# Performance work log

Hardware: AMD Instinct MI355X
Metric: run time of the kernel (lower is better)

The kernel has to match this reference:

```python
import jax, jax.numpy as jnp
import numpy as np

N_NODES = 100000
N_EDGES = 1600000
DIM_IN = 128
DIM_OUT = 64


def _spmm(edge_row, edge_col, edge_vals, X):
    # DAD.mm(X): sparse COO [N,N] times dense [N,d]
    # gather source features, scale by edge value, scatter-add to rows
    msgs = edge_vals[:, None] * X[edge_col]          # [E, d]
    return jax.ops.segment_sum(msgs, edge_row, num_segments=N_NODES)


def setup_inputs() -> dict:
    key = jax.random.key(0)
    k1, k2, k3, k4, k5, k6 = jax.random.split(key, 6)
    X = jax.random.normal(k1, (N_NODES, DIM_IN), dtype=jnp.float32)
    W1 = jax.random.normal(k2, (DIM_IN, DIM_IN), dtype=jnp.float32) * (1.0 / np.sqrt(DIM_IN))
    W2 = jax.random.normal(k3, (DIM_OUT, DIM_IN), dtype=jnp.float32) * (1.0 / np.sqrt(DIM_IN))
    edge_vals = jax.random.uniform(k4, (N_EDGES,), dtype=jnp.float32)
    edge_row = jax.random.randint(k5, (N_EDGES,), 0, N_NODES, dtype=jnp.int32)
    edge_col = jax.random.randint(k6, (N_EDGES,), 0, N_NODES, dtype=jnp.int32)
    return {"X": X, "W1": W1, "W2": W2, "edge_vals": edge_vals,
            "edge_row": edge_row, "edge_col": edge_col}


def reference(X, W1, W2, edge_vals, edge_row, edge_col):
    # layer 1: tanh(fc1(DAD @ X)); nn.Linear(bias=False) is x @ W.T
    h = jnp.tanh(_spmm(edge_row, edge_col, edge_vals, X) @ W1.T)
    # layer 2: tanh(fc2(DAD @ h))
    out = jnp.tanh(_spmm(edge_row, edge_col, edge_vals, h) @ W2.T)
    return out
```

## Files before the change

### kernel.cpp

```cpp
#include <hip/hip_runtime.h>
#include <hip/hip_bf16.h>
#include <hip/hip_fp16.h>

#define N_NODES 100000
#define N_EDGES 1600000
#define DIM_IN 128
#define DIM_OUT 64

#define NB 391
#define NCHUNK 391
#define CHUNK 4096
#define BCAP 5120

typedef unsigned int uint;
typedef unsigned short ushort;
typedef _Float16 half8 __attribute__((ext_vector_type(8)));
typedef float f32x4 __attribute__((ext_vector_type(4)));

__device__ inline ushort f2h(float f) {
    __half h = __float2half(f);
    return *reinterpret_cast<ushort*>(&h);
}


__global__ __launch_bounds__(256) void chunk_hist_kernel(const int* __restrict__ erow,
                                                         int* __restrict__ counts, int E) {
    __shared__ int hist[NB];
    const int t = threadIdx.x, c = blockIdx.x;
    for (int b = t; b < NB; b += 256) hist[b] = 0;
    __syncthreads();
    const int eb = c * CHUNK;
#pragma unroll
    for (int i = 0; i < CHUNK / 256; ++i) {
        int e = eb + i * 256 + t;
        if (e < E) atomicAdd(&hist[erow[e] >> 8], 1);
    }
    __syncthreads();
    for (int b = t; b < NB; b += 256) counts[b * NCHUNK + c] = hist[b];
}

__global__ __launch_bounds__(512) void bucket_scan_kernel(const int* __restrict__ counts,
                                                          int* __restrict__ offnb,
                                                          int* __restrict__ tot) {
    __shared__ int s[512];
    const int b = blockIdx.x, t = threadIdx.x;
    int v = (t < NCHUNK) ? counts[b * NCHUNK + t] : 0;
    s[t] = v;
    __syncthreads();
#pragma unroll
    for (int o = 1; o < 512; o <<= 1) {
        int x = s[t];
        int y = (t >= o) ? s[t - o] : 0;
        __syncthreads();
        s[t] = x + y;
        __syncthreads();
    }
    if (t < NCHUNK) offnb[b * NCHUNK + t] = s[t] - v;
    if (t == 511) tot[b] = s[511];
}

__global__ __launch_bounds__(512) void base_scan_kernel(const int* __restrict__ tot,
                                                        int* __restrict__ bbase) {
    __shared__ int s[512];
    const int t = threadIdx.x;
    int v = (t < NB) ? tot[t] : 0;
    s[t] = v;
    __syncthreads();
#pragma unroll
    for (int o = 1; o < 512; o <<= 1) {
        int x = s[t];
        int y = (t >= o) ? s[t - o] : 0;
        __syncthreads();
        s[t] = x + y;
        __syncthreads();
    }
    if (t < NB) bbase[t] = s[t] - v;
    if (t == 511) bbase[NB] = s[511];
}

__global__ __launch_bounds__(512) void coarse_scatter_kernel(const int* __restrict__ erow,
                                                             const int* __restrict__ ecol,
                                                             const float* __restrict__ eval,
                                                             const int* __restrict__ offnb,
                                                             const int* __restrict__ bbase,
                                                             uint* __restrict__ keyOut,
                                                             float* __restrict__ valOut, int E) {
    __shared__ int hist[NB];
    __shared__ int segOff[NB];
    __shared__ int localOff[NB];
    __shared__ int sc[512];
    __shared__ int idxL[CHUNK];
    __shared__ int gaddrL[CHUNK];

    const int t = threadIdx.x, c = blockIdx.x;
    for (int b = t; b < NB; b += 512) {
        hist[b] = 0;
        segOff[b] = bbase[b] + offnb[b * NCHUNK + c];
    }
    __syncthreads();
    const int eb = c * CHUNK;
    uint bq[CHUNK / 512];
#pragma unroll
    for (int i = 0; i < CHUNK / 512; ++i) {
        int e = eb + i * 512 + t;
        if (e < E) {
            int b = erow[e] >> 8;
            int q = atomicAdd(&hist[b], 1);
            bq[i] = ((uint)b << 16) | (uint)q;
        } else {
            bq[i] = 0xFFFFFFFFu;
        }
    }
    __syncthreads();
    int v = (t < NB) ? hist[t] : 0;
    sc[t] = v;
    __syncthreads();
#pragma unroll
    for (int o = 1; o < 512; o <<= 1) {
        int x = sc[t];
        int y = (t >= o) ? sc[t - o] : 0;
        __syncthreads();
        sc[t] = x + y;
        __syncthreads();
    }
    if (t < NB) localOff[t] = sc[t] - v;
    __syncthreads();
#pragma unroll
    for (int i = 0; i < CHUNK / 512; ++i) {
        if (bq[i] != 0xFFFFFFFFu) {
            int b = bq[i] >> 16;
            int q = bq[i] & 0xFFFF;
            int s = localOff[b] + q;
            idxL[s] = eb + i * 512 + t;
            gaddrL[s] = segOff[b] + q;
        }
    }
    __syncthreads();
    const int m = min(CHUNK, E - eb);
    for (int s = t; s < m; s += 512) {
        int e = idxL[s];
        int g = gaddrL[s];
        keyOut[g] = ((uint)(erow[e] & 255) << 17) | (uint)ecol[e];
        valOut[g] = eval[e];
    }
}

__global__ __launch_bounds__(256) void fine_sort_kernel(const uint* __restrict__ keyOut,
                                                        const float* __restrict__ valOut,
                                                        const int* __restrict__ bbase,
                                                        int* __restrict__ row_ptr,
                                                        int2* __restrict__ ep) {
    __shared__ uint keyL[BCAP];
    __shared__ int hist[256];
    __shared__ int offs[256];
    const int b = blockIdx.x, t = threadIdx.x;
    const int s0 = bbase[b], s1 = bbase[b + 1];
    const int m = min(s1 - s0, BCAP);
    hist[t] = 0;
    __syncthreads();
    for (int j = t; j < m; j += 256) {
        uint k = keyOut[s0 + j];
        keyL[j] = k;
        atomicAdd(&hist[k >> 17], 1);
    }
    __syncthreads();
    int v = hist[t];
    offs[t] = v;
    __syncthreads();
#pragma unroll
    for (int o = 1; o < 256; o <<= 1) {
        int x = offs[t];
        int y = (t >= o) ? offs[t - o] : 0;
        __syncthreads();
        offs[t] = x + y;
        __syncthreads();
    }
    int excl = offs[t] - v;
    int row = b * 256 + t;
    if (row < N_NODES) row_ptr[row] = s0 + excl;
    if (b == NB - 1 && t == 0) row_ptr[N_NODES] = s1;
    hist[t] = excl;
    __syncthreads();
    for (int j = t; j < m; j += 256) {
        uint k = keyL[j];
        int pos = atomicAdd(&hist[k >> 17], 1);
        float vv = valOut[s0 + j];
        ep[s0 + pos] = make_int2((int)(k & 0x1FFFFu), __float_as_int(vv));
    }
}


__global__ __launch_bounds__(256) void cvt_f16_kernel(const float* __restrict__ in,
                                                      uint* __restrict__ outp, int n8) {
    int i = blockIdx.x * 256 + threadIdx.x;
    if (i >= n8) return;
    const float4* in4 = reinterpret_cast<const float4*>(in) + (size_t)i * 2;
    float4 a = in4[0];
    float4 b = in4[1];
    uint4 o;
    o.x = (uint)f2h(a.x) | ((uint)f2h(a.y) << 16);
    o.y = (uint)f2h(a.z) | ((uint)f2h(a.w) << 16);
    o.z = (uint)f2h(b.x) | ((uint)f2h(b.y) << 16);
    o.w = (uint)f2h(b.z) | ((uint)f2h(b.w) << 16);
    reinterpret_cast<uint4*>(outp)[i] = o;
}


__global__ __launch_bounds__(256) void spmm_f16_kernel(const int2* __restrict__ ep,
                                                       const int* __restrict__ row_ptr,
                                                       const uint* __restrict__ Xh,
                                                       uint* __restrict__ aggh) {
    int wave = threadIdx.x >> 6;
    int lane = threadIdx.x & 63;
    int r = blockIdx.x * 4 + wave;
    if (r >= N_NODES) return;
    int beg = row_ptr[r];
    int end = row_ptr[r + 1];
    float a0x = 0.f, a0y = 0.f, a1x = 0.f, a1y = 0.f;
    int e = beg;
    for (; e + 7 < end; e += 8) {
        int2 cv[8];
        uint xu[8];
#pragma unroll
        for (int i = 0; i < 8; ++i) cv[i] = ep[e + i];
#pragma unroll
        for (int i = 0; i < 8; ++i) xu[i] = Xh[(size_t)cv[i].x * 64 + lane];
#pragma unroll
        for (int i = 0; i < 8; ++i) {
            float v = __int_as_float(cv[i].y);
            __half2 h2 = *reinterpret_cast<__half2*>(&xu[i]);
            float2 f = __half22float2(h2);
            if (i & 1) { a1x += v * f.x; a1y += v * f.y; }
            else       { a0x += v * f.x; a0y += v * f.y; }
        }
    }
    for (; e < end; ++e) {
        int2 cv = ep[e];
        float v = __int_as_float(cv.y);
        uint xu = Xh[(size_t)cv.x * 64 + lane];
        __half2 h2 = *reinterpret_cast<__half2*>(&xu);
        float2 f = __half22float2(h2);
        a0x += v * f.x;
        a0y += v * f.y;
    }
    uint o = (uint)f2h(a0x + a1x) | ((uint)f2h(a0y + a1y) << 16);
    aggh[(size_t)r * 64 + lane] = o;
}


__global__ __launch_bounds__(256) void spmm64_f16_tanh_kernel(const int2* __restrict__ ep,
                                                              const int* __restrict__ row_ptr,
                                                              const ushort* __restrict__ Ph,
                                                              float* __restrict__ out) {
    int wave = threadIdx.x >> 6;
    int lane = threadIdx.x & 63;
    int r = blockIdx.x * 4 + wave;
    if (r >= N_NODES) return;
    int beg = row_ptr[r];
    int end = row_ptr[r + 1];
    float acc0 = 0.f, acc1 = 0.f;
    int e = beg;
    for (; e + 7 < end; e += 8) {
        int2 cv[8];
        ushort xu[8];
#pragma unroll
        for (int i = 0; i < 8; ++i) cv[i] = ep[e + i];
#pragma unroll
        for (int i = 0; i < 8; ++i) xu[i] = Ph[(size_t)cv[i].x * 64 + lane];
#pragma unroll
        for (int i = 0; i < 8; ++i) {
            float v = __int_as_float(cv[i].y);
            __half h = *reinterpret_cast<__half*>(&xu[i]);
            float x = __half2float(h);
            if (i & 1) acc1 += v * x;
            else       acc0 += v * x;
        }
    }
    for (; e < end; ++e) {
        int2 cv = ep[e];
        ushort u = Ph[(size_t)cv.x * 64 + lane];
        __half h = *reinterpret_cast<__half*>(&u);
        acc0 += __int_as_float(cv.y) * __half2float(h);
    }
    out[(size_t)r * DIM_OUT + lane] = tanhf(acc0 + acc1);
}


__global__ __launch_bounds__(256) void fused_mlp_kernel(const uint* __restrict__ Ah,
                                                        const uint* __restrict__ W1h,
                                                        const uint* __restrict__ W2h,
                                                        uint* __restrict__ Ph, int M) {
    __shared__ __align__(16) ushort sA[128 * 128];
    __shared__ __align__(16) ushort sW1[128 * 128];
    __shared__ __align__(16) ushort sW2[64 * 128];

    const int t = threadIdx.x;
    const int l = t & 63;
    const int w = t >> 6;
    const int row0 = blockIdx.x * 128;
    const int lr = l & 15;
    const int lk = l >> 4;

#pragma unroll
    for (int i = 0; i < 8; ++i) {
        int fid = i * 256 + t;
        int row = fid >> 4, slot = fid & 15;
        int gr = row0 + row;
        uint4 v = make_uint4(0, 0, 0, 0);
        if (gr < M) v = reinterpret_cast<const uint4*>(Ah)[(size_t)gr * 16 + slot];
        *reinterpret_cast<uint4*>(&sA[row * 128 + ((slot ^ (row & 7)) << 3)]) = v;
    }
#pragma unroll
    for (int i = 0; i < 8; ++i) {
        int fid = i * 256 + t;
        int row = fid >> 4, slot = fid & 15;
        uint4 v = reinterpret_cast<const uint4*>(W1h)[row * 16 + slot];
        *reinterpret_cast<uint4*>(&sW1[row * 128 + ((slot ^ (row & 7)) << 3)]) = v;
    }
#pragma unroll
    for (int i = 0; i < 4; ++i) {
        int fid = i * 256 + t;
        int row = fid >> 4, slot = fid & 15;
        uint4 v = reinterpret_cast<const uint4*>(W2h)[row * 16 + slot];
        *reinterpret_cast<uint4*>(&sW2[row * 128 + ((slot ^ (row & 7)) << 3)]) = v;
    }
    __syncthreads();

    f32x4 acc[2][8];
#pragma unroll
    for (int rf = 0; rf < 2; ++rf)
#pragma unroll
        for (int cf = 0; cf < 8; ++cf) acc[rf][cf] = (f32x4){0.f, 0.f, 0.f, 0.f};

    half8 aF[2][4];
#pragma unroll
    for (int rf = 0; rf < 2; ++rf) {
        int row = w * 32 + rf * 16 + lr;
#pragma unroll
        for (int kc = 0; kc < 4; ++kc) {
            int slot = kc * 4 + lk;
            aF[rf][kc] = *reinterpret_cast<const half8*>(&sA[row * 128 + ((slot ^ (row & 7)) << 3)]);
        }
    }
#pragma unroll
    for (int cf = 0; cf < 8; ++cf) {
        int col = cf * 16 + lr;
#pragma unroll
        for (int kc = 0; kc < 4; ++kc) {
            int slot = kc * 4 + lk;
            half8 bF = *reinterpret_cast<const half8*>(&sW1[col * 128 + ((slot ^ (col & 7)) << 3)]);
            acc[0][cf] = __builtin_amdgcn_mfma_f32_16x16x32_f16(aF[0][kc], bF, acc[0][cf], 0, 0, 0);
            acc[1][cf] = __builtin_amdgcn_mfma_f32_16x16x32_f16(aF[1][kc], bF, acc[1][cf], 0, 0, 0);
        }
    }
    __syncthreads();

#pragma unroll
    for (int rf = 0; rf < 2; ++rf)
#pragma unroll
        for (int cf = 0; cf < 8; ++cf)
#pragma unroll
            for (int reg = 0; reg < 4; ++reg) {
                int row = w * 32 + rf * 16 + lk * 4 + reg;
                int col = cf * 16 + lr;
                sA[row * 128 + (((col >> 3) ^ (row & 7)) << 3) + (col & 7)] =
                    f2h(tanhf(acc[rf][cf][reg]));
            }
    __syncthreads();

    f32x4 acc2[2][4];
#pragma unroll
    for (int rf = 0; rf < 2; ++rf)
#pragma unroll
        for (int cf = 0; cf < 4; ++cf) acc2[rf][cf] = (f32x4){0.f, 0.f, 0.f, 0.f};
#pragma unroll
    for (int rf = 0; rf < 2; ++rf) {
        int row = w * 32 + rf * 16 + lr;
#pragma unroll
        for (int kc = 0; kc < 4; ++kc) {
            int slot = kc * 4 + lk;
            aF[rf][kc] = *reinterpret_cast<const half8*>(&sA[row * 128 + ((slot ^ (row & 7)) << 3)]);
        }
    }
#pragma unroll
    for (int cf = 0; cf < 4; ++cf) {
        int col = cf * 16 + lr;
#pragma unroll
        for (int kc = 0; kc < 4; ++kc) {
            int slot = kc * 4 + lk;
            half8 bF = *reinterpret_cast<const half8*>(&sW2[col * 128 + ((slot ^ (col & 7)) << 3)]);
            acc2[0][cf] = __builtin_amdgcn_mfma_f32_16x16x32_f16(aF[0][kc], bF, acc2[0][cf], 0, 0, 0);
            acc2[1][cf] = __builtin_amdgcn_mfma_f32_16x16x32_f16(aF[1][kc], bF, acc2[1][cf], 0, 0, 0);
        }
    }

    ushort* sP = sW1;
#pragma unroll
    for (int rf = 0; rf < 2; ++rf)
#pragma unroll
        for (int cf = 0; cf < 4; ++cf)
#pragma unroll
            for (int reg = 0; reg < 4; ++reg) {
                int row = w * 32 + rf * 16 + lk * 4 + reg;
                int col = cf * 16 + lr;
                sP[row * 64 + col] = f2h(acc2[rf][cf][reg]);
            }
    __syncthreads();

#pragma unroll
    for (int i = 0; i < 4; ++i) {
        int fid = i * 256 + t;
        int row = fid >> 3, q = fid & 7;
        int gr = row0 + row;
        if (gr < M)
            reinterpret_cast<uint4*>(Ph)[(size_t)gr * 8 + q] =
                *reinterpret_cast<const uint4*>(&sP[row * 64 + q * 8]);
    }
}


extern "C" void kernel_launch(void* const* d_in, const int* in_sizes, int n_in,
                              void* d_out, int out_size, void* d_ws, size_t ws_size,
                              hipStream_t stream) {
    const float* X = (const float*)d_in[0];
    const float* W1 = (const float*)d_in[1];
    const float* W2 = (const float*)d_in[2];
    const float* evals = (const float*)d_in[3];
    const int* erow = (const int*)d_in[4];
    const int* ecol = (const int*)d_in[5];
    float* out = (float*)d_out;

    const int N = N_NODES;
    const int E = N_EDGES;

    char* ws = (char*)d_ws;
    size_t off = 0;
    auto alloc = [&](size_t bytes) {
        size_t o = off;
        off = (off + bytes + 255) & ~(size_t)255;
        return o;
    };
    size_t o_counts = alloc((size_t)NB * NCHUNK * 4);
    size_t o_offnb = alloc((size_t)NB * NCHUNK * 4);
    size_t o_tot = alloc((size_t)NB * 4);
    size_t o_bbase = alloc((size_t)(NB + 1) * 4);
    size_t o_rowptr = alloc((size_t)(N + 1) * 4);
    size_t o_ep = alloc((size_t)E * 8);
    size_t o_agg = alloc((size_t)N * 64 * 4);
    size_t o_xh = alloc((size_t)N * 64 * 4);
    size_t o_p = alloc((size_t)N * 32 * 4);
    size_t o_w1h = alloc((size_t)128 * 64 * 4);
    size_t o_w2h = alloc((size_t)64 * 64 * 4);
    (void)ws_size;

    int* counts = (int*)(ws + o_counts);
    int* offnb = (int*)(ws + o_offnb);
    int* tot = (int*)(ws + o_tot);
    int* bbase = (int*)(ws + o_bbase);
    int* row_ptr = (int*)(ws + o_rowptr);
    int2* ep = (int2*)(ws + o_ep);
    uint* aggh = (uint*)(ws + o_agg);
    uint* Xh = (uint*)(ws + o_xh);
    uint* Ph = (uint*)(ws + o_p);
    uint* W1h = (uint*)(ws + o_w1h);
    uint* W2h = (uint*)(ws + o_w2h);
    uint* keyOut = (uint*)(ws + o_agg);
    float* valOut = (float*)(ws + o_agg + (size_t)E * 4);

    const int ncvt = N * DIM_IN / 8;
    cvt_f16_kernel<<<(ncvt + 255) / 256, 256, 0, stream>>>(X, Xh, ncvt);
    cvt_f16_kernel<<<8, 256, 0, stream>>>(W1, W1h, 128 * 128 / 8);
    cvt_f16_kernel<<<4, 256, 0, stream>>>(W2, W2h, 64 * 128 / 8);

    chunk_hist_kernel<<<NCHUNK, 256, 0, stream>>>(erow, counts, E);
    bucket_scan_kernel<<<NB, 512, 0, stream>>>(counts, offnb, tot);
    base_scan_kernel<<<1, 512, 0, stream>>>(tot, bbase);
    coarse_scatter_kernel<<<NCHUNK, 512, 0, stream>>>(erow, ecol, evals, offnb, bbase,
                                                      keyOut, valOut, E);
    fine_sort_kernel<<<NB, 256, 0, stream>>>(keyOut, valOut, bbase, row_ptr, ep);

    const int spmm_grid = (N + 3) / 4;
    const int mlp_grid = (N + 127) / 128;

    spmm_f16_kernel<<<spmm_grid, 256, 0, stream>>>(ep, row_ptr, Xh, aggh);
    fused_mlp_kernel<<<mlp_grid, 256, 0, stream>>>(aggh, W1h, W2h, Ph, N);
    spmm64_f16_tanh_kernel<<<spmm_grid, 256, 0, stream>>>(ep, row_ptr, (const ushort*)Ph, out);
}
```

Before: 240.0 us.

## Reassociate layer one to transform before aggregating, fusing the fp32-to-fp16 cast into the GEMM

Layer one now computes X·W1ᵀ first with an MFMA GEMM that reads the fp32 X directly and converts it to fp16 while loading, which drops the separate X conversion kernel. The SpMM then aggregates the transformed features and applies tanh in its epilogue. The fused two-layer MLP is split into two templated GEMM launches: the first replaces the X cast, the second applies W2 to the aggregated hidden features. The SpMM kernels also replace their scalar tail loop with a predicated 8-wide loop and add an early exit for empty rows. The trade-off is an extra full-size hidden-activation buffer written and read between kernels, plus separate key/value scratch buffers.

```diff
diff --git a/kernel.cpp b/kernel.cpp
--- a/kernel.cpp
+++ b/kernel.cpp
@@ -206,216 +206,186 @@
 }
 
 
-__global__ __launch_bounds__(256) void spmm_f16_kernel(const int2* __restrict__ ep,
-                                                       const int* __restrict__ row_ptr,
-                                                       const uint* __restrict__ Xh,
-                                                       uint* __restrict__ aggh) {
+template <int NOUT, bool TANH, bool AF32>
+__global__ __launch_bounds__(256) void mfma_gemm_kernel(const void* __restrict__ Ain,
+                                                        const uint* __restrict__ Wh,
+                                                        uint* __restrict__ Out, int M) {
+    constexpr int CF = NOUT / 16;
+    __shared__ __align__(16) ushort sA[128 * 128];
+    __shared__ __align__(16) ushort sB[NOUT * 128];
+
+    const int t = threadIdx.x;
+    const int l = t & 63;
+    const int w = t >> 6;
+    const int row0 = blockIdx.x * 128;
+    const int lr = l & 15;
+    const int lk = l >> 4;
+
+    if (AF32) {
+        const float* Af = (const float*)Ain;
+#pragma unroll
+        for (int i = 0; i < 16; ++i) {
+            int fid = i * 256 + t;
+            int row = fid >> 5, q4 = fid & 31;
+            int gr = row0 + row;
+            float4 v = make_float4(0.f, 0.f, 0.f, 0.f);
+            if (gr < M) v = *reinterpret_cast<const float4*>(Af + (size_t)gr * 128 + q4 * 4);
+            uint2 p;
+            p.x = (uint)f2h(v.x) | ((uint)f2h(v.y) << 16);
+            p.y = (uint)f2h(v.z) | ((uint)f2h(v.w) << 16);
+            int slot = q4 >> 1;
+            *reinterpret_cast<uint2*>(&sA[row * 128 + ((slot ^ (row & 7)) << 3) + (q4 & 1) * 4]) = p;
+        }
+    } else {
+        const uint4* A4 = (const uint4*)Ain;
+#pragma unroll
+        for (int i = 0; i < 8; ++i) {
+            int fid = i * 256 + t;
+            int row = fid >> 4, slot = fid & 15;
+            int gr = row0 + row;
+            uint4 v = make_uint4(0, 0, 0, 0);
+            if (gr < M) v = A4[(size_t)gr * 16 + slot];
+            *reinterpret_cast<uint4*>(&sA[row * 128 + ((slot ^ (row & 7)) << 3)]) = v;
+        }
+    }
+#pragma unroll
+    for (int i = 0; i < NOUT / 16; ++i) {
+        int fid = i * 256 + t;
+        int row = fid >> 4, slot = fid & 15;
+        uint4 v = reinterpret_cast<const uint4*>(Wh)[row * 16 + slot];
+        *reinterpret_cast<uint4*>(&sB[row * 128 + ((slot ^ (row & 7)) << 3)]) = v;
+    }
+    __syncthreads();
+
+    f32x4 acc[2][CF];
+#pragma unroll
+    for (int rf = 0; rf < 2; ++rf)
+#pragma unroll
+        for (int cf = 0; cf < CF; ++cf) acc[rf][cf] = (f32x4){0.f, 0.f, 0.f, 0.f};
+
+    half8 aF[2][4];
+#pragma unroll
+    for (int rf = 0; rf < 2; ++rf) {
+        int row = w * 32 + rf * 16 + lr;
+#pragma unroll
+        for (int kc = 0; kc < 4; ++kc) {
+            int slot = kc * 4 + lk;
+            aF[rf][kc] = *reinterpret_cast<const half8*>(&sA[row * 128 + ((slot ^ (row & 7)) << 3)]);
+        }
+    }
+#pragma unroll
+    for (int cf = 0; cf < CF; ++cf) {
+        int col = cf * 16 + lr;
+#pragma unroll
+        for (int kc = 0; kc < 4; ++kc) {
+            int slot = kc * 4 + lk;
+            half8 bF = *reinterpret_cast<const half8*>(&sB[col * 128 + ((slot ^ (col & 7)) << 3)]);
+            acc[0][cf] = __builtin_amdgcn_mfma_f32_16x16x32_f16(aF[0][kc], bF, acc[0][cf], 0, 0, 0);
+            acc[1][cf] = __builtin_amdgcn_mfma_f32_16x16x32_f16(aF[1][kc], bF, acc[1][cf], 0, 0, 0);
+        }
+    }
+    __syncthreads();
+
+    ushort* sOut = sA;
+#pragma unroll
+    for (int rf = 0; rf < 2; ++rf)
+#pragma unroll
+        for (int cf = 0; cf < CF; ++cf)
+#pragma unroll
+            for (int reg = 0; reg < 4; ++reg) {
+                int row = w * 32 + rf * 16 + lk * 4 + reg;
+                int col = cf * 16 + lr;
+                float x = acc[rf][cf][reg];
+                sOut[row * NOUT + col] = f2h(TANH ? tanhf(x) : x);
+            }
+    __syncthreads();
+    constexpr int QPR = NOUT / 8;
+#pragma unroll
+    for (int i = 0; i < 128 * QPR / 256; ++i) {
+        int fid = i * 256 + t;
+        int row = fid / QPR, q = fid % QPR;
+        int gr = row0 + row;
+        if (gr < M)
+            reinterpret_cast<uint4*>(Out)[(size_t)gr * QPR + q] =
+                *reinterpret_cast<const uint4*>(&sOut[row * NOUT + q * 8]);
+    }
+}
+
+
+__global__ __launch_bounds__(256) void spmm1_kernel(const int2* __restrict__ ep,
+                                                    const int* __restrict__ row_ptr,
+                                                    const uint* __restrict__ T,
+                                                    uint* __restrict__ Hh) {
     int wave = threadIdx.x >> 6;
     int lane = threadIdx.x & 63;
     int r = blockIdx.x * 4 + wave;
     if (r >= N_NODES) return;
     int beg = row_ptr[r];
     int end = row_ptr[r + 1];
+    if (beg >= end) {
+        Hh[(size_t)r * 64 + lane] = 0u;
+        return;
+    }
     float a0x = 0.f, a0y = 0.f, a1x = 0.f, a1y = 0.f;
-    int e = beg;
-    for (; e + 7 < end; e += 8) {
+    for (int e = beg; e < end; e += 8) {
         int2 cv[8];
         uint xu[8];
 #pragma unroll
-        for (int i = 0; i < 8; ++i) cv[i] = ep[e + i];
-#pragma unroll
-        for (int i = 0; i < 8; ++i) xu[i] = Xh[(size_t)cv[i].x * 64 + lane];
-#pragma unroll
         for (int i = 0; i < 8; ++i) {
-            float v = __int_as_float(cv[i].y);
+            int idx = (e + i < end) ? e + i : end - 1;
+            cv[i] = ep[idx];
+        }
+#pragma unroll
+        for (int i = 0; i < 8; ++i) xu[i] = T[(size_t)cv[i].x * 64 + lane];
+#pragma unroll
+        for (int i = 0; i < 8; ++i) {
+            float v = (e + i < end) ? __int_as_float(cv[i].y) : 0.f;
             __half2 h2 = *reinterpret_cast<__half2*>(&xu[i]);
             float2 f = __half22float2(h2);
             if (i & 1) { a1x += v * f.x; a1y += v * f.y; }
             else       { a0x += v * f.x; a0y += v * f.y; }
         }
     }
-    for (; e < end; ++e) {
-        int2 cv = ep[e];
-        float v = __int_as_float(cv.y);
-        uint xu = Xh[(size_t)cv.x * 64 + lane];
-        __half2 h2 = *reinterpret_cast<__half2*>(&xu);
-        float2 f = __half22float2(h2);
-        a0x += v * f.x;
-        a0y += v * f.y;
-    }
-    uint o = (uint)f2h(a0x + a1x) | ((uint)f2h(a0y + a1y) << 16);
-    aggh[(size_t)r * 64 + lane] = o;
-}
-
-
-__global__ __launch_bounds__(256) void spmm64_f16_tanh_kernel(const int2* __restrict__ ep,
-                                                              const int* __restrict__ row_ptr,
-                                                              const ushort* __restrict__ Ph,
-                                                              float* __restrict__ out) {
+    Hh[(size_t)r * 64 + lane] =
+        (uint)f2h(tanhf(a0x + a1x)) | ((uint)f2h(tanhf(a0y + a1y)) << 16);
+}
+
+
+__global__ __launch_bounds__(256) void spmm2_kernel(const int2* __restrict__ ep,
+                                                    const int* __restrict__ row_ptr,
+                                                    const ushort* __restrict__ Ph,
+                                                    float* __restrict__ out) {
     int wave = threadIdx.x >> 6;
     int lane = threadIdx.x & 63;
     int r = blockIdx.x * 4 + wave;
     if (r >= N_NODES) return;
     int beg = row_ptr[r];
     int end = row_ptr[r + 1];
+    if (beg >= end) {
+        out[(size_t)r * DIM_OUT + lane] = 0.f;
+        return;
+    }
     float acc0 = 0.f, acc1 = 0.f;
-    int e = beg;
-    for (; e + 7 < end; e += 8) {
+    for (int e = beg; e < end; e += 8) {
         int2 cv[8];
         ushort xu[8];
 #pragma unroll
-        for (int i = 0; i < 8; ++i) cv[i] = ep[e + i];
+        for (int i = 0; i < 8; ++i) {
+            int idx = (e + i < end) ? e + i : end - 1;
+            cv[i] = ep[idx];
+        }
 #pragma unroll
         for (int i = 0; i < 8; ++i) xu[i] = Ph[(size_t)cv[i].x * 64 + lane];
 #pragma unroll
         for (int i = 0; i < 8; ++i) {
-            float v = __int_as_float(cv[i].y);
+            float v = (e + i < end) ? __int_as_float(cv[i].y) : 0.f;
             __half h = *reinterpret_cast<__half*>(&xu[i]);
             float x = __half2float(h);
             if (i & 1) acc1 += v * x;
             else       acc0 += v * x;
         }
     }
-    for (; e < end; ++e) {
-        int2 cv = ep[e];
-        ushort u = Ph[(size_t)cv.x * 64 + lane];
-        __half h = *reinterpret_cast<__half*>(&u);
-        acc0 += __int_as_float(cv.y) * __half2float(h);
-    }
     out[(size_t)r * DIM_OUT + lane] = tanhf(acc0 + acc1);
-}
-
-
-__global__ __launch_bounds__(256) void fused_mlp_kernel(const uint* __restrict__ Ah,
-                                                        const uint* __restrict__ W1h,
-                                                        const uint* __restrict__ W2h,
-                                                        uint* __restrict__ Ph, int M) {
-    __shared__ __align__(16) ushort sA[128 * 128];
-    __shared__ __align__(16) ushort sW1[128 * 128];
-    __shared__ __align__(16) ushort sW2[64 * 128];
-
-    const int t = threadIdx.x;
-    const int l = t & 63;
-    const int w = t >> 6;
-    const int row0 = blockIdx.x * 128;
-    const int lr = l & 15;
-    const int lk = l >> 4;
-
-#pragma unroll
-    for (int i = 0; i < 8; ++i) {
-        int fid = i * 256 + t;
-        int row = fid >> 4, slot = fid & 15;
-        int gr = row0 + row;
-        uint4 v = make_uint4(0, 0, 0, 0);
-        if (gr < M) v = reinterpret_cast<const uint4*>(Ah)[(size_t)gr * 16 + slot];
-        *reinterpret_cast<uint4*>(&sA[row * 128 + ((slot ^ (row & 7)) << 3)]) = v;
-    }
-#pragma unroll
-    for (int i = 0; i < 8; ++i) {
-        int fid = i * 256 + t;
-        int row = fid >> 4, slot = fid & 15;
-        uint4 v = reinterpret_cast<const uint4*>(W1h)[row * 16 + slot];
-        *reinterpret_cast<uint4*>(&sW1[row * 128 + ((slot ^ (row & 7)) << 3)]) = v;
-    }
-#pragma unroll
-    for (int i = 0; i < 4; ++i) {
-        int fid = i * 256 + t;
-        int row = fid >> 4, slot = fid & 15;
-        uint4 v = reinterpret_cast<const uint4*>(W2h)[row * 16 + slot];
-        *reinterpret_cast<uint4*>(&sW2[row * 128 + ((slot ^ (row & 7)) << 3)]) = v;
-    }
-    __syncthreads();
-
-    f32x4 acc[2][8];
-#pragma unroll
-    for (int rf = 0; rf < 2; ++rf)
-#pragma unroll
-        for (int cf = 0; cf < 8; ++cf) acc[rf][cf] = (f32x4){0.f, 0.f, 0.f, 0.f};
-
-    half8 aF[2][4];
-#pragma unroll
-    for (int rf = 0; rf < 2; ++rf) {
-        int row = w * 32 + rf * 16 + lr;
-#pragma unroll
-        for (int kc = 0; kc < 4; ++kc) {
-            int slot = kc * 4 + lk;
-            aF[rf][kc] = *reinterpret_cast<const half8*>(&sA[row * 128 + ((slot ^ (row & 7)) << 3)]);
-        }
-    }
-#pragma unroll
-    for (int cf = 0; cf < 8; ++cf) {
-        int col = cf * 16 + lr;
-#pragma unroll
-        for (int kc = 0; kc < 4; ++kc) {
-            int slot = kc * 4 + lk;
-            half8 bF = *reinterpret_cast<const half8*>(&sW1[col * 128 + ((slot ^ (col & 7)) << 3)]);
-            acc[0][cf] = __builtin_amdgcn_mfma_f32_16x16x32_f16(aF[0][kc], bF, acc[0][cf], 0, 0, 0);
-            acc[1][cf] = __builtin_amdgcn_mfma_f32_16x16x32_f16(aF[1][kc], bF, acc[1][cf], 0, 0, 0);
-        }
-    }
-    __syncthreads();
-
-#pragma unroll
-    for (int rf = 0; rf < 2; ++rf)
-#pragma unroll
-        for (int cf = 0; cf < 8; ++cf)
-#pragma unroll
-            for (int reg = 0; reg < 4; ++reg) {
-                int row = w * 32 + rf * 16 + lk * 4 + reg;
-                int col = cf * 16 + lr;
-                sA[row * 128 + (((col >> 3) ^ (row & 7)) << 3) + (col & 7)] =
-                    f2h(tanhf(acc[rf][cf][reg]));
-            }
-    __syncthreads();
-
-    f32x4 acc2[2][4];
-#pragma unroll
-    for (int rf = 0; rf < 2; ++rf)
-#pragma unroll
-        for (int cf = 0; cf < 4; ++cf) acc2[rf][cf] = (f32x4){0.f, 0.f, 0.f, 0.f};
-#pragma unroll
-    for (int rf = 0; rf < 2; ++rf) {
-        int row = w * 32 + rf * 16 + lr;
-#pragma unroll
-        for (int kc = 0; kc < 4; ++kc) {
-            int slot = kc * 4 + lk;
-            aF[rf][kc] = *reinterpret_cast<const half8*>(&sA[row * 128 + ((slot ^ (row & 7)) << 3)]);
-        }
-    }
-#pragma unroll
-    for (int cf = 0; cf < 4; ++cf) {
-        int col = cf * 16 + lr;
-#pragma unroll
-        for (int kc = 0; kc < 4; ++kc) {
-            int slot = kc * 4 + lk;
-            half8 bF = *reinterpret_cast<const half8*>(&sW2[col * 128 + ((slot ^ (col & 7)) << 3)]);
-            acc2[0][cf] = __builtin_amdgcn_mfma_f32_16x16x32_f16(aF[0][kc], bF, acc2[0][cf], 0, 0, 0);
-            acc2[1][cf] = __builtin_amdgcn_mfma_f32_16x16x32_f16(aF[1][kc], bF, acc2[1][cf], 0, 0, 0);
-        }
-    }
-
-    ushort* sP = sW1;
-#pragma unroll
-    for (int rf = 0; rf < 2; ++rf)
-#pragma unroll
-        for (int cf = 0; cf < 4; ++cf)
-#pragma unroll
-            for (int reg = 0; reg < 4; ++reg) {
-                int row = w * 32 + rf * 16 + lk * 4 + reg;
-                int col = cf * 16 + lr;
-                sP[row * 64 + col] = f2h(acc2[rf][cf][reg]);
-            }
-    __syncthreads();
-
-#pragma unroll
-    for (int i = 0; i < 4; ++i) {
-        int fid = i * 256 + t;
-        int row = fid >> 3, q = fid & 7;
-        int gr = row0 + row;
-        if (gr < M)
-            reinterpret_cast<uint4*>(Ph)[(size_t)gr * 8 + q] =
-                *reinterpret_cast<const uint4*>(&sP[row * 64 + q * 8]);
-    }
 }
 
 
@@ -446,9 +416,11 @@
     size_t o_bbase = alloc((size_t)(NB + 1) * 4);
     size_t o_rowptr = alloc((size_t)(N + 1) * 4);
     size_t o_ep = alloc((size_t)E * 8);
-    size_t o_agg = alloc((size_t)N * 64 * 4);
-    size_t o_xh = alloc((size_t)N * 64 * 4);
-    size_t o_p = alloc((size_t)N * 32 * 4);
+    size_t o_key = alloc((size_t)E * 4);
+    size_t o_val = alloc((size_t)E * 4);
+    size_t o_xw1 = alloc((size_t)N * 64 * 4);
+    size_t o_hh = alloc((size_t)N * 64 * 4);
+    size_t o_ph = alloc((size_t)N * 32 * 4);
     size_t o_w1h = alloc((size_t)128 * 64 * 4);
     size_t o_w2h = alloc((size_t)64 * 64 * 4);
     (void)ws_size;
@@ -459,18 +431,20 @@
     int* bbase = (int*)(ws + o_bbase);
     int* row_ptr = (int*)(ws + o_rowptr);
     int2* ep = (int2*)(ws + o_ep);
-    uint* aggh = (uint*)(ws + o_agg);
-    uint* Xh = (uint*)(ws + o_xh);
-    uint* Ph = (uint*)(ws + o_p);
+    uint* keyOut = (uint*)(ws + o_key);
+    float* valOut = (float*)(ws + o_val);
+    uint* XW1h = (uint*)(ws + o_xw1);
+    uint* Hh = (uint*)(ws + o_hh);
+    uint* Ph = (uint*)(ws + o_ph);
     uint* W1h = (uint*)(ws + o_w1h);
     uint* W2h = (uint*)(ws + o_w2h);
-    uint* keyOut = (uint*)(ws + o_agg);
-    float* valOut = (float*)(ws + o_agg + (size_t)E * 4);
-
-    const int ncvt = N * DIM_IN / 8;
-    cvt_f16_kernel<<<(ncvt + 255) / 256, 256, 0, stream>>>(X, Xh, ncvt);
+
+    const int gemm_grid = (N + 127) / 128;
+    const int spmm_grid = (N + 3) / 4;
+
     cvt_f16_kernel<<<8, 256, 0, stream>>>(W1, W1h, 128 * 128 / 8);
     cvt_f16_kernel<<<4, 256, 0, stream>>>(W2, W2h, 64 * 128 / 8);
+    mfma_gemm_kernel<128, false, true><<<gemm_grid, 256, 0, stream>>>(X, W1h, XW1h, N);
 
     chunk_hist_kernel<<<NCHUNK, 256, 0, stream>>>(erow, counts, E);
     bucket_scan_kernel<<<NB, 512, 0, stream>>>(counts, offnb, tot);
@@ -479,10 +453,7 @@
                                                       keyOut, valOut, E);
     fine_sort_kernel<<<NB, 256, 0, stream>>>(keyOut, valOut, bbase, row_ptr, ep);
 
-    const int spmm_grid = (N + 3) / 4;
-    const int mlp_grid = (N + 127) / 128;
-
-    spmm_f16_kernel<<<spmm_grid, 256, 0, stream>>>(ep, row_ptr, Xh, aggh);
-    fused_mlp_kernel<<<mlp_grid, 256, 0, stream>>>(aggh, W1h, W2h, Ph, N);
-    spmm64_f16_tanh_kernel<<<spmm_grid, 256, 0, stream>>>(ep, row_ptr, (const ushort*)Ph, out);
-}
+    spmm1_kernel<<<spmm_grid, 256, 0, stream>>>(ep, row_ptr, XW1h, Hh);
+    mfma_gemm_kernel<64, false, false><<<gemm_grid, 256, 0, stream>>>(Hh, W2h, Ph, N);
+    spmm2_kernel<<<spmm_grid, 256, 0, stream>>>(ep, row_ptr, (const ushort*)Ph, out);
+}
```

Result: no change. 244.6 us (+1.9%).
